# Kernel tuning notes

Hardware: AMD Instinct MI355X
Metric: run time of the kernel (lower is better)

## Reference

```python
import jax, jax.numpy as jnp
import numpy as np
import math

IN_DIM = 256
OUT_DIM = 256
MAX_IN = 1024
MAX_OUT = 512
BATCH = 2
SEQ = 1024  # actual_seq_len == max_in_seq here
RED = 2
LN_EPS = 1e-5


def setup_inputs() -> dict:
    key = jax.random.key(0)
    ks = jax.random.split(key, 8)
    N = BATCH * SEQ
    return {
        "x": jax.random.normal(ks[0], (N, IN_DIM), dtype=jnp.float32),
        "M": jax.random.uniform(ks[1], (OUT_DIM, IN_DIM), minval=-0.5, maxval=0.5, dtype=jnp.float32),
        "P": jax.random.uniform(ks[2], (OUT_DIM, OUT_DIM), minval=-0.1, maxval=0.1, dtype=jnp.float32),
        "Linker": jax.random.uniform(ks[3], (MAX_IN, MAX_OUT), minval=-0.1, maxval=0.1, dtype=jnp.float32),
        "ln_gamma": jnp.ones((OUT_DIM,), dtype=jnp.float32),
        "ln_beta": jnp.zeros((OUT_DIM,), dtype=jnp.float32),
        "res_W": jax.random.uniform(ks[4], (OUT_DIM, IN_DIM), minval=-0.1, maxval=0.1, dtype=jnp.float32),
        "res_linker": jax.random.uniform(ks[5], (MAX_IN, MAX_OUT), minval=-0.1, maxval=0.1, dtype=jnp.float32),
        "actual_seq_len": SEQ,
    }


def _layer_norm(z, gamma, beta):
    mu = jnp.mean(z, axis=-1, keepdims=True)
    var = jnp.mean((z - mu) ** 2, axis=-1, keepdims=True)
    return (z - mu) * jax.lax.rsqrt(var + LN_EPS) * gamma + beta


def _periods():
    i = jnp.arange(OUT_DIM, dtype=jnp.float32)[:, None]
    j = jnp.arange(OUT_DIM, dtype=jnp.float32)[None, :]
    return i * OUT_DIM + j + 2.0  # (D, D)


def reference(x, M, P, Linker, ln_gamma, ln_beta, res_W, res_linker, actual_seq_len):
    S = int(actual_seq_len)
    N, _ = x.shape
    B = N // S
    D = OUT_DIM
    out_seq = max(1, S // RED)

    # Z = LN(x @ M^T)
    Z = _layer_norm(x @ M.T, ln_gamma, ln_beta)  # (N, D)

    # position transform: T[k,i] = sum_j Z[k,j] * P[i,j] * cos(2*pi*k / periods[i,j])
    k = jnp.arange(N, dtype=jnp.float32)[:, None, None]  # (N,1,1)
    phi = jnp.cos(2.0 * math.pi * k / _periods()[None])   # (N, D, D)
    T = jnp.einsum('kj,ij,kij->ki', Z, P, phi)            # (N, D)

    # adaptive sequence-length transform via Linker slice
    L = Linker[:S, :out_seq]                               # (S, out_seq)
    U = jnp.einsum('bsd,st->btd', T.reshape(B, S, D), L).reshape(B * out_seq, D)

    # 'separate' residual path
    rfeat = (x @ res_W.T).reshape(B, S, D)
    rL = res_linker[:S, :out_seq]
    residual = jnp.einsum('bsd,st->btd', rfeat, rL).reshape(B * out_seq, D)

    return U + residual
```

## Files before the change

kernel.cpp:

```cpp
#include <hip/hip_runtime.h>

#define D256 256
#define KT 8
#define S_SEQ 1024
#define OUTSEQ 512

__global__ __launch_bounds__(256) void k_prep(const float* __restrict__ M,
                                              const float* __restrict__ resW,
                                              const float* __restrict__ P,
                                              float2* __restrict__ MW,
                                              float4* __restrict__ PIt4) {
  const int j = blockIdx.x;
  const int t = threadIdx.x;
  MW[j * D256 + t] = make_float2(M[t * D256 + j], resW[t * D256 + j]);
  const float p = (float)(t * D256 + j + 2);
  const float ip = 1.0f / p;
  const float cb2 = 2.0f * __builtin_amdgcn_cosf(ip);
  PIt4[j * D256 + t] = make_float4(P[t * D256 + j], ip, cb2, 0.0f);
}

__global__ __launch_bounds__(1024, 4) void k_AB(const float* __restrict__ x,
                                                const float2* __restrict__ MW,
                                                const float4* __restrict__ PIt4,
                                                const float* __restrict__ gamma,
                                                const float* __restrict__ beta,
                                                float* __restrict__ T,
                                                float* __restrict__ rfeat) {
  __shared__ float Xs[D256][12];
  __shared__ float red[4][KT][D256];
  __shared__ float mu_s[KT], rs_s[KT];
  const int tid = threadIdx.x;
  const int i = tid & 255;
  const int h = tid >> 8;
  const int j0 = h * 64;
  const int k0 = blockIdx.x * KT;

  Xs[i][h]     = x[(k0 + h) * D256 + i];
  Xs[i][h + 4] = x[(k0 + h + 4) * D256 + i];
  __syncthreads();

  float aM[KT], aR[KT];
  #pragma unroll
  for (int r = 0; r < KT; ++r) { aM[r] = 0.f; aR[r] = 0.f; }
  {
    const float2* mwp = MW + i;
    #pragma unroll 8
    for (int jj = 0; jj < 64; ++jj) {
      const int j = j0 + jj;
      const float2 mw = mwp[j * D256];
      const float4 z0 = *(const float4*)&Xs[j][0];
      const float4 z1 = *(const float4*)&Xs[j][4];
      aM[0] = fmaf(z0.x, mw.x, aM[0]); aR[0] = fmaf(z0.x, mw.y, aR[0]);
      aM[1] = fmaf(z0.y, mw.x, aM[1]); aR[1] = fmaf(z0.y, mw.y, aR[1]);
      aM[2] = fmaf(z0.z, mw.x, aM[2]); aR[2] = fmaf(z0.z, mw.y, aR[2]);
      aM[3] = fmaf(z0.w, mw.x, aM[3]); aR[3] = fmaf(z0.w, mw.y, aR[3]);
      aM[4] = fmaf(z1.x, mw.x, aM[4]); aR[4] = fmaf(z1.x, mw.y, aR[4]);
      aM[5] = fmaf(z1.y, mw.x, aM[5]); aR[5] = fmaf(z1.y, mw.y, aR[5]);
      aM[6] = fmaf(z1.z, mw.x, aM[6]); aR[6] = fmaf(z1.z, mw.y, aR[6]);
      aM[7] = fmaf(z1.w, mw.x, aM[7]); aR[7] = fmaf(z1.w, mw.y, aR[7]);
    }
  }

  #pragma unroll
  for (int r = 0; r < KT; ++r) red[h][r][i] = aR[r];
  __syncthreads();
  #pragma unroll
  for (int p = 0; p < 2; ++p) {
    const int r = h * 2 + p;
    rfeat[(k0 + r) * D256 + i] =
        red[0][r][i] + red[1][r][i] + red[2][r][i] + red[3][r][i];
  }
  __syncthreads();

  #pragma unroll
  for (int r = 0; r < KT; ++r) red[h][r][i] = aM[r];
  __syncthreads();
  #pragma unroll
  for (int p = 0; p < 2; ++p) {
    const int r = h * 2 + p;
    Xs[i][r] = red[0][r][i] + red[1][r][i] + red[2][r][i] + red[3][r][i];
  }
  __syncthreads();

  const int w = tid >> 6, lane = tid & 63;
  if (w < KT) {
    float s = 0.f, sq = 0.f;
    #pragma unroll
    for (int l = 0; l < 4; ++l) {
      const float v = Xs[lane + 64 * l][w];
      s += v;
      sq = fmaf(v, v, sq);
    }
    #pragma unroll
    for (int off = 32; off; off >>= 1) {
      s += __shfl_down(s, off);
      sq += __shfl_down(sq, off);
    }
    if (lane == 0) {
      const float m = s * (1.0f / 256.0f);
      const float var = sq * (1.0f / 256.0f) - m * m;
      mu_s[w] = m;
      rs_s[w] = rsqrtf(var + 1e-5f);
    }
  }
  __syncthreads();
  {
    const float g = gamma[i], be = beta[i];
    #pragma unroll
    for (int p = 0; p < 2; ++p) {
      const int r = h + 4 * p;
      Xs[i][r] = (Xs[i][r] - mu_s[r]) * rs_s[r] * g + be;
    }
  }
  __syncthreads();

  float accT[KT] = {};
  const float kf0 = (float)k0, kf1 = (float)(k0 + 1);
  {
    const float4* pip = PIt4 + i;
    #pragma unroll 4
    for (int jj = 0; jj < 64; ++jj) {
      const int j = j0 + jj;
      const float4 pi = pip[j * D256];
      const float4 z0 = *(const float4*)&Xs[j][0];
      const float4 z1 = *(const float4*)&Xs[j][4];
      float r0 = kf0 * pi.y; r0 -= floorf(r0);
      float r1 = kf1 * pi.y; r1 -= floorf(r1);
      float c0 = __builtin_amdgcn_cosf(r0);
      float c1 = __builtin_amdgcn_cosf(r1);
      accT[0] = fmaf(z0.x * pi.x, c0, accT[0]);
      accT[1] = fmaf(z0.y * pi.x, c1, accT[1]);
      float c2;
      c2 = fmaf(pi.z, c1, -c0); accT[2] = fmaf(z0.z * pi.x, c2, accT[2]); c0 = c1; c1 = c2;
      c2 = fmaf(pi.z, c1, -c0); accT[3] = fmaf(z0.w * pi.x, c2, accT[3]); c0 = c1; c1 = c2;
      c2 = fmaf(pi.z, c1, -c0); accT[4] = fmaf(z1.x * pi.x, c2, accT[4]); c0 = c1; c1 = c2;
      c2 = fmaf(pi.z, c1, -c0); accT[5] = fmaf(z1.y * pi.x, c2, accT[5]); c0 = c1; c1 = c2;
      c2 = fmaf(pi.z, c1, -c0); accT[6] = fmaf(z1.z * pi.x, c2, accT[6]); c0 = c1; c1 = c2;
      c2 = fmaf(pi.z, c1, -c0); accT[7] = fmaf(z1.w * pi.x, c2, accT[7]);
    }
  }
  #pragma unroll
  for (int r = 0; r < KT; ++r) red[h][r][i] = accT[r];
  __syncthreads();
  #pragma unroll
  for (int p = 0; p < 2; ++p) {
    const int r = h * 2 + p;
    T[(k0 + r) * D256 + i] =
        red[0][r][i] + red[1][r][i] + red[2][r][i] + red[3][r][i];
  }
}

__global__ __launch_bounds__(256) void k_C1(const float* __restrict__ T,
                                            const float* __restrict__ rfeat,
                                            const float* __restrict__ Linker,
                                            const float* __restrict__ rLinker,
                                            float* __restrict__ part) {
  __shared__ float Ls[128][8];
  __shared__ float rLs[128][8];
  const int bid = blockIdx.x;
  const int sc = bid & 7;
  const int tt = (bid >> 3) & 63;
  const int b  = bid >> 9;
  const int t0 = tt * 8;
  const int s0 = sc * 128;
  const int d  = threadIdx.x;

  {
    const int row = threadIdx.x >> 1;
    const int c4  = (threadIdx.x & 1) * 4;
    *(float4*)&Ls[row][c4]  = *(const float4*)&Linker[(s0 + row) * OUTSEQ + t0 + c4];
    *(float4*)&rLs[row][c4] = *(const float4*)&rLinker[(s0 + row) * OUTSEQ + t0 + c4];
  }
  __syncthreads();

  float acc[8] = {};
  const float* Tp = &T[(b * S_SEQ + s0) * D256 + d];
  const float* Rp = &rfeat[(b * S_SEQ + s0) * D256 + d];
  #pragma unroll 4
  for (int s = 0; s < 128; ++s) {
    const float tv = Tp[s * D256];
    const float rv = Rp[s * D256];
    const float4 l0 = *(const float4*)&Ls[s][0];
    const float4 l1 = *(const float4*)&Ls[s][4];
    const float4 r0 = *(const float4*)&rLs[s][0];
    const float4 r1 = *(const float4*)&rLs[s][4];
    acc[0] = fmaf(tv, l0.x, acc[0]); acc[0] = fmaf(rv, r0.x, acc[0]);
    acc[1] = fmaf(tv, l0.y, acc[1]); acc[1] = fmaf(rv, r0.y, acc[1]);
    acc[2] = fmaf(tv, l0.z, acc[2]); acc[2] = fmaf(rv, r0.z, acc[2]);
    acc[3] = fmaf(tv, l0.w, acc[3]); acc[3] = fmaf(rv, r0.w, acc[3]);
    acc[4] = fmaf(tv, l1.x, acc[4]); acc[4] = fmaf(rv, r1.x, acc[4]);
    acc[5] = fmaf(tv, l1.y, acc[5]); acc[5] = fmaf(rv, r1.y, acc[5]);
    acc[6] = fmaf(tv, l1.z, acc[6]); acc[6] = fmaf(rv, r1.z, acc[6]);
    acc[7] = fmaf(tv, l1.w, acc[7]); acc[7] = fmaf(rv, r1.w, acc[7]);
  }

  const int rowbase = b * 512 + t0;
  #pragma unroll
  for (int u = 0; u < 8; ++u)
    part[(((sc << 10) + rowbase + u) << 8) + d] = acc[u];
}

__global__ __launch_bounds__(256) void k_C2(const float* __restrict__ part,
                                            float* __restrict__ out) {
  const int row = blockIdx.x;
  const int d   = threadIdx.x;
  float s = 0.f;
  #pragma unroll
  for (int sc = 0; sc < 8; ++sc)
    s += part[(((sc << 10) + row) << 8) + d];
  out[(row << 8) + d] = s;
}

extern "C" void kernel_launch(void* const* d_in, const int* in_sizes, int n_in,
                              void* d_out, int out_size, void* d_ws, size_t ws_size,
                              hipStream_t stream) {
  const float* x       = (const float*)d_in[0];
  const float* M       = (const float*)d_in[1];
  const float* P       = (const float*)d_in[2];
  const float* Linker  = (const float*)d_in[3];
  const float* gamma   = (const float*)d_in[4];
  const float* beta    = (const float*)d_in[5];
  const float* resW    = (const float*)d_in[6];
  const float* rLinker = (const float*)d_in[7];
  float* out = (float*)d_out;

  char* ws = (char*)d_ws;
  float2* MW    = (float2*)(ws);
  float4* PIt4  = (float4*)(ws + 512 * 1024);
  float*  T     = (float*)(ws + 1536 * 1024);
  float*  rfeat = (float*)(ws + 3584 * 1024);
  float*  part  = (float*)(ws + 5632 * 1024);

  hipLaunchKernelGGL(k_prep, dim3(256),  dim3(256),  0, stream, M, resW, P, MW, PIt4);
  hipLaunchKernelGGL(k_AB,   dim3(256),  dim3(1024), 0, stream, x, MW, PIt4, gamma, beta, T, rfeat);
  hipLaunchKernelGGL(k_C1,   dim3(1024), dim3(256),  0, stream, T, rfeat, Linker, rLinker, part);
  hipLaunchKernelGGL(k_C2,   dim3(1024), dim3(256),  0, stream, part, out);
}
```

Measured before the change: 61.59 us.

## Run sequence-linker contraction on bf16 MFMA with transposed bf16 operands

Replaces the scalar FP32 linker contraction with a bf16 MFMA (16x16x32) GEMM. k_prep transposes and converts Linker and res_linker to bf16, and k_AB writes T and rfeat transposed as bf16 into one concatenated K dimension, so the two einsums become a single GEMM with K=2048 split into 8 chunks and summed by a reduction kernel. It also uses the hardware fract instruction for range reduction in the cosine loop. This lowers FP32 FMA and memory traffic in the contraction stage but rounds T, rfeat and the linkers to bf16, which may hurt accuracy.

Result: faster. 49.78 us (-19.2%).

```diff
diff --git a/kernel.cpp b/kernel.cpp
--- a/kernel.cpp
+++ b/kernel.cpp
@@ -5,18 +5,65 @@
 #define S_SEQ 1024
 #define OUTSEQ 512
 
+typedef __attribute__((ext_vector_type(8))) short bf16x8;
+typedef __attribute__((ext_vector_type(8))) unsigned short u16x8;
+typedef __attribute__((ext_vector_type(4))) float f32x4;
+
+__device__ inline unsigned short f2bf(float f) {
+  unsigned u = __float_as_uint(f);
+  return (unsigned short)((u + 0x7fffu + ((u >> 16) & 1u)) >> 16);
+}
+
 __global__ __launch_bounds__(256) void k_prep(const float* __restrict__ M,
                                               const float* __restrict__ resW,
                                               const float* __restrict__ P,
+                                              const float* __restrict__ Linker,
+                                              const float* __restrict__ rLinker,
                                               float2* __restrict__ MW,
-                                              float4* __restrict__ PIt4) {
-  const int j = blockIdx.x;
-  const int t = threadIdx.x;
-  MW[j * D256 + t] = make_float2(M[t * D256 + j], resW[t * D256 + j]);
-  const float p = (float)(t * D256 + j + 2);
-  const float ip = 1.0f / p;
-  const float cb2 = 2.0f * __builtin_amdgcn_cosf(ip);
-  PIt4[j * D256 + t] = make_float4(P[t * D256 + j], ip, cb2, 0.0f);
+                                              float4* __restrict__ PIt4,
+                                              unsigned short* __restrict__ LinkTb) {
+  __shared__ float tl[64][65];
+  const int tid = threadIdx.x;
+  if (blockIdx.x < 256) {
+    const int j = blockIdx.x;
+    const int t = tid;
+    MW[j * D256 + t] = make_float2(M[t * D256 + j], resW[t * D256 + j]);
+    const float p = (float)(t * D256 + j + 2);
+    const float ip = 1.0f / p;
+    const float cb2 = 2.0f * __builtin_amdgcn_cosf(ip);
+    PIt4[j * D256 + t] = make_float4(P[t * D256 + j], ip, cb2, 0.0f);
+    return;
+  }
+  const int tb = blockIdx.x - 256;
+  const int st = tb & 31;
+  const int tt = tb >> 5;
+  const int s0 = st * 64, t0 = tt * 64;
+  const float* src = (s0 < 1024) ? (Linker + (size_t)s0 * OUTSEQ)
+                                 : (rLinker + (size_t)(s0 - 1024) * OUTSEQ);
+  {
+    const int sy = tid >> 2, sx = tid & 3;
+    #pragma unroll
+    for (int c = 0; c < 4; ++c) {
+      const int ci = sx + c * 4;
+      const float4 v = *(const float4*)&src[sy * OUTSEQ + t0 + ci * 4];
+      tl[ci * 4 + 0][sy] = v.x;
+      tl[ci * 4 + 1][sy] = v.y;
+      tl[ci * 4 + 2][sy] = v.z;
+      tl[ci * 4 + 3][sy] = v.w;
+    }
+  }
+  __syncthreads();
+  {
+    const int ty = tid >> 2, tx = tid & 3;
+    u16x8 o0, o1;
+    #pragma unroll
+    for (int e = 0; e < 8; ++e) o0[e] = f2bf(tl[ty][tx * 16 + e]);
+    #pragma unroll
+    for (int e = 0; e < 8; ++e) o1[e] = f2bf(tl[ty][tx * 16 + 8 + e]);
+    unsigned short* dst = LinkTb + (size_t)(t0 + ty) * 2048 + s0 + tx * 16;
+    *(u16x8*)dst = o0;
+    *(u16x8*)(dst + 8) = o1;
+  }
 }
 
 __global__ __launch_bounds__(1024, 4) void k_AB(const float* __restrict__ x,
@@ -24,8 +71,7 @@
                                                 const float4* __restrict__ PIt4,
                                                 const float* __restrict__ gamma,
                                                 const float* __restrict__ beta,
-                                                float* __restrict__ T,
-                                                float* __restrict__ rfeat) {
+                                                unsigned short* __restrict__ Bt) {
   __shared__ float Xs[D256][12];
   __shared__ float red[4][KT][D256];
   __shared__ float mu_s[KT], rs_s[KT];
@@ -64,11 +110,12 @@
   #pragma unroll
   for (int r = 0; r < KT; ++r) red[h][r][i] = aR[r];
   __syncthreads();
-  #pragma unroll
-  for (int p = 0; p < 2; ++p) {
-    const int r = h * 2 + p;
-    rfeat[(k0 + r) * D256 + i] =
-        red[0][r][i] + red[1][r][i] + red[2][r][i] + red[3][r][i];
+  if (tid < 256) {
+    u16x8 o;
+    #pragma unroll
+    for (int r = 0; r < KT; ++r)
+      o[r] = f2bf(red[0][r][tid] + red[1][r][tid] + red[2][r][tid] + red[3][r][tid]);
+    *(u16x8*)(Bt + (size_t)tid * 4096 + 2048 + k0) = o;
   }
   __syncthreads();
 
@@ -124,8 +171,8 @@
       const float4 pi = pip[j * D256];
       const float4 z0 = *(const float4*)&Xs[j][0];
       const float4 z1 = *(const float4*)&Xs[j][4];
-      float r0 = kf0 * pi.y; r0 -= floorf(r0);
-      float r1 = kf1 * pi.y; r1 -= floorf(r1);
+      const float r0 = __builtin_amdgcn_fractf(kf0 * pi.y);
+      const float r1 = __builtin_amdgcn_fractf(kf1 * pi.y);
       float c0 = __builtin_amdgcn_cosf(r0);
       float c1 = __builtin_amdgcn_cosf(r1);
       accT[0] = fmaf(z0.x * pi.x, c0, accT[0]);
@@ -142,73 +189,72 @@
   #pragma unroll
   for (int r = 0; r < KT; ++r) red[h][r][i] = accT[r];
   __syncthreads();
-  #pragma unroll
-  for (int p = 0; p < 2; ++p) {
-    const int r = h * 2 + p;
-    T[(k0 + r) * D256 + i] =
-        red[0][r][i] + red[1][r][i] + red[2][r][i] + red[3][r][i];
-  }
-}
-
-__global__ __launch_bounds__(256) void k_C1(const float* __restrict__ T,
-                                            const float* __restrict__ rfeat,
-                                            const float* __restrict__ Linker,
-                                            const float* __restrict__ rLinker,
+  if (tid < 256) {
+    u16x8 o;
+    #pragma unroll
+    for (int r = 0; r < KT; ++r)
+      o[r] = f2bf(red[0][r][tid] + red[1][r][tid] + red[2][r][tid] + red[3][r][tid]);
+    *(u16x8*)(Bt + (size_t)tid * 4096 + k0) = o;
+  }
+}
+
+__global__ __launch_bounds__(256) void k_Cm(const unsigned short* __restrict__ LinkTb,
+                                            const unsigned short* __restrict__ Bt,
                                             float* __restrict__ part) {
-  __shared__ float Ls[128][8];
-  __shared__ float rLs[128][8];
   const int bid = blockIdx.x;
-  const int sc = bid & 7;
-  const int tt = (bid >> 3) & 63;
-  const int b  = bid >> 9;
-  const int t0 = tt * 8;
-  const int s0 = sc * 128;
-  const int d  = threadIdx.x;
-
-  {
-    const int row = threadIdx.x >> 1;
-    const int c4  = (threadIdx.x & 1) * 4;
-    *(float4*)&Ls[row][c4]  = *(const float4*)&Linker[(s0 + row) * OUTSEQ + t0 + c4];
-    *(float4*)&rLs[row][c4] = *(const float4*)&rLinker[(s0 + row) * OUTSEQ + t0 + c4];
-  }
-  __syncthreads();
-
-  float acc[8] = {};
-  const float* Tp = &T[(b * S_SEQ + s0) * D256 + d];
-  const float* Rp = &rfeat[(b * S_SEQ + s0) * D256 + d];
-  #pragma unroll 4
-  for (int s = 0; s < 128; ++s) {
-    const float tv = Tp[s * D256];
-    const float rv = Rp[s * D256];
-    const float4 l0 = *(const float4*)&Ls[s][0];
-    const float4 l1 = *(const float4*)&Ls[s][4];
-    const float4 r0 = *(const float4*)&rLs[s][0];
-    const float4 r1 = *(const float4*)&rLs[s][4];
-    acc[0] = fmaf(tv, l0.x, acc[0]); acc[0] = fmaf(rv, r0.x, acc[0]);
-    acc[1] = fmaf(tv, l0.y, acc[1]); acc[1] = fmaf(rv, r0.y, acc[1]);
-    acc[2] = fmaf(tv, l0.z, acc[2]); acc[2] = fmaf(rv, r0.z, acc[2]);
-    acc[3] = fmaf(tv, l0.w, acc[3]); acc[3] = fmaf(rv, r0.w, acc[3]);
-    acc[4] = fmaf(tv, l1.x, acc[4]); acc[4] = fmaf(rv, r1.x, acc[4]);
-    acc[5] = fmaf(tv, l1.y, acc[5]); acc[5] = fmaf(rv, r1.y, acc[5]);
-    acc[6] = fmaf(tv, l1.z, acc[6]); acc[6] = fmaf(rv, r1.z, acc[6]);
-    acc[7] = fmaf(tv, l1.w, acc[7]); acc[7] = fmaf(rv, r1.w, acc[7]);
-  }
-
-  const int rowbase = b * 512 + t0;
-  #pragma unroll
-  for (int u = 0; u < 8; ++u)
-    part[(((sc << 10) + rowbase + u) << 8) + d] = acc[u];
-}
-
-__global__ __launch_bounds__(256) void k_C2(const float* __restrict__ part,
-                                            float* __restrict__ out) {
+  const int kc = bid & 7;
+  const int dt = (bid >> 3) & 3;
+  const int tt = (bid >> 5) & 7;
+  const int b  = bid >> 8;
+  const int wv = threadIdx.x >> 6;
+  const int l  = threadIdx.x & 63;
+  const int wm = wv >> 1, wn = wv & 1;
+  const int t0 = tt * 64 + wm * 32;
+  const int d0 = dt * 64 + wn * 32;
+  const int m  = l & 15;
+  const int q  = l >> 4;
+  const int sc0 = kc * 128;
+
+  f32x4 acc00 = {}, acc01 = {}, acc10 = {}, acc11 = {};
+  const unsigned short* Arow = LinkTb + (size_t)(t0 + m) * 2048;
+  const unsigned short* Brow = Bt + (size_t)(d0 + m) * 4096;
+
+  #pragma unroll
+  for (int seg = 0; seg < 2; ++seg) {
+    const int acol = seg * 1024 + sc0 + q * 8;
+    const int bcol = seg * 2048 + b * 1024 + sc0 + q * 8;
+    #pragma unroll
+    for (int ks = 0; ks < 4; ++ks) {
+      const bf16x8 a0 = *(const bf16x8*)(Arow + acol + ks * 32);
+      const bf16x8 a1 = *(const bf16x8*)(Arow + 16 * 2048 + acol + ks * 32);
+      const bf16x8 b0 = *(const bf16x8*)(Brow + bcol + ks * 32);
+      const bf16x8 b1 = *(const bf16x8*)(Brow + 16 * 4096 + bcol + ks * 32);
+      acc00 = __builtin_amdgcn_mfma_f32_16x16x32_bf16(a0, b0, acc00, 0, 0, 0);
+      acc01 = __builtin_amdgcn_mfma_f32_16x16x32_bf16(a0, b1, acc01, 0, 0, 0);
+      acc10 = __builtin_amdgcn_mfma_f32_16x16x32_bf16(a1, b0, acc10, 0, 0, 0);
+      acc11 = __builtin_amdgcn_mfma_f32_16x16x32_bf16(a1, b1, acc11, 0, 0, 0);
+    }
+  }
+
+  float* pb = part + ((size_t)kc << 18) + (size_t)(b * 512 + t0 + q * 4) * D256 + d0 + m;
+  #pragma unroll
+  for (int reg = 0; reg < 4; ++reg) {
+    pb[(0 + reg) * D256 + 0]       = acc00[reg];
+    pb[(0 + reg) * D256 + 16]      = acc01[reg];
+    pb[(16 + reg) * D256 + 0]      = acc10[reg];
+    pb[(16 + reg) * D256 + 16]     = acc11[reg];
+  }
+}
+
+__global__ __launch_bounds__(256) void k_Cred(const float* __restrict__ part,
+                                              float* __restrict__ out) {
   const int row = blockIdx.x;
   const int d   = threadIdx.x;
   float s = 0.f;
   #pragma unroll
-  for (int sc = 0; sc < 8; ++sc)
-    s += part[(((sc << 10) + row) << 8) + d];
-  out[(row << 8) + d] = s;
+  for (int kc = 0; kc < 8; ++kc)
+    s += part[((size_t)kc << 18) + row * D256 + d];
+  out[row * D256 + d] = s;
 }
 
 extern "C" void kernel_launch(void* const* d_in, const int* in_sizes, int n_in,
@@ -225,14 +271,16 @@
   float* out = (float*)d_out;
 
   char* ws = (char*)d_ws;
-  float2* MW    = (float2*)(ws);
-  float4* PIt4  = (float4*)(ws + 512 * 1024);
-  float*  T     = (float*)(ws + 1536 * 1024);
-  float*  rfeat = (float*)(ws + 3584 * 1024);
-  float*  part  = (float*)(ws + 5632 * 1024);
-
-  hipLaunchKernelGGL(k_prep, dim3(256),  dim3(256),  0, stream, M, resW, P, MW, PIt4);
-  hipLaunchKernelGGL(k_AB,   dim3(256),  dim3(1024), 0, stream, x, MW, PIt4, gamma, beta, T, rfeat);
-  hipLaunchKernelGGL(k_C1,   dim3(1024), dim3(256),  0, stream, T, rfeat, Linker, rLinker, part);
-  hipLaunchKernelGGL(k_C2,   dim3(1024), dim3(256),  0, stream, part, out);
-}
+  float2*         MW     = (float2*)(ws);
+  float4*         PIt4   = (float4*)(ws + 512 * 1024);
+  unsigned short* LinkTb = (unsigned short*)(ws + 1536 * 1024);
+  unsigned short* Bt     = (unsigned short*)(ws + 3584 * 1024);
+  float*          part   = (float*)(ws + 5632 * 1024);
+
+  hipLaunchKernelGGL(k_prep, dim3(512),  dim3(256),  0, stream,
+                     M, resW, P, Linker, rLinker, MW, PIt4, LinkTb);
+  hipLaunchKernelGGL(k_AB,   dim3(256),  dim3(1024), 0, stream,
+                     x, MW, PIt4, gamma, beta, Bt);
+  hipLaunchKernelGGL(k_Cm,   dim3(512),  dim3(256),  0, stream, LinkTb, Bt, part);
+  hipLaunchKernelGGL(k_Cred, dim3(1024), dim3(256),  0, stream, part, out);
+}
```
